# Optimization experiments

Measured on AMD Instinct MI355X. Metric: run time of the kernel, lower is better.

Reference implementation:

```python
import jax, jax.numpy as jnp
import numpy as np

B, L, D = 2, 2048, 1024
H, Z = 16, 64  # n_heads, head_dim


def setup_inputs() -> dict:
    key = jax.random.key(0)
    k1, k2, k3 = jax.random.split(key, 3)
    scale = 1.0 / np.sqrt(D)  # keep projections O(1) for numeric sanity
    x = jax.random.normal(k1, (B, L, D), dtype=jnp.float32)
    Wq = jax.random.normal(k2, (H, Z, D), dtype=jnp.float32) * scale
    Wk = jax.random.normal(k3, (H, Z, D), dtype=jnp.float32) * scale
    beta = jnp.ones((1,), dtype=jnp.float32) / jnp.sqrt(jnp.float32(Z))  # default beta = 1/sqrt(head_dim)
    return {"x": x, "Wq": Wq, "Wk": Wk, "beta": beta}


def _energy(x, Wq, Wk, beta):
    # x: (b, l, d); Wq/Wk: (h, z, d); beta: (1,)
    kp = jnp.einsum('bld,hzd->blhz', x, Wk)
    qp = jnp.einsum('bld,hzd->blhz', x, Wq)
    b0 = beta[0]
    # attention[b,h,q,k] = beta * <k_proj[b,q,h], q_proj[b,k,h]>  (faithful to original index order)
    att = b0 * jnp.einsum('bqhz,bkhz->bhqk', kp, qp)
    e = jax.nn.logsumexp(att, axis=-1)          # (b, h, q)
    e = e.sum(axis=-1).sum(axis=-1)             # (b,)
    return (-1.0 / b0) * e


def reference(x, Wq, Wk, beta):
    # value_and_grad: forward returns (energy, d(energy.sum)/dx)
    def esum(xx):
        return _energy(xx, Wq, Wk, beta).sum()
    en = _energy(x, Wq, Wk, beta)               # (b,)
    gx = jax.grad(esum)(x)                      # (b, l, d)
    return en, gx
```

## Files before the change

kernel.cpp:

```cpp
#include <hip/hip_runtime.h>
#include <math.h>

#define L 2048
#define D 1024
#define H 16
#define Z 64
#define HZ 1024

typedef __bf16 bf16x8 __attribute__((ext_vector_type(8)));
typedef float f32x4 __attribute__((ext_vector_type(4)));
typedef float f32x16 __attribute__((ext_vector_type(16)));

#if __has_builtin(__builtin_amdgcn_exp2f)
#define EXP2(x) __builtin_amdgcn_exp2f(x)
#else
#define EXP2(x) exp2f(x)
#endif

__device__ __forceinline__ void async_ld16(const void* g, void* l) {
  __builtin_amdgcn_global_load_lds(
      (const __attribute__((address_space(1))) uint32_t*)(uintptr_t)g,
      (__attribute__((address_space(3))) uint32_t*)(uint32_t)(uintptr_t)l,
      16, 0, 0);
}

template<int NPIECE>
__device__ __forceinline__ void stage_async(const __bf16* __restrict__ g,
                                            int gstride, char* lds, int tid) {
  const int l = tid & 63, w = tid >> 6;
#pragma unroll
  for (int it = 0; it < NPIECE; ++it) {
    const int region = it * 4 + w;
    const int r = ((region >> 1) << 4) + (l & 15);
    const int c = ((region & 1) << 2) + (l >> 4);
    async_ld16(g + (size_t)r * gstride + c * 8, lds + (region << 10));
  }
}

__device__ __forceinline__ bf16x8 rfrag(const char* lds, int row, int cc) {
  const int region = ((row >> 4) << 1) + (cc >> 2);
  const int slot = (row & 15) + ((cc & 3) << 4);
  return *(const bf16x8*)(lds + region * 1024 + slot * 16);
}

__global__ __launch_bounds__(256) void cvt_kernel(const float* __restrict__ s,
                                                  __bf16* __restrict__ d, int n4) {
  int i = blockIdx.x * 256 + threadIdx.x;
  if (i < n4) {
    float4 v = ((const float4*)s)[i];
    union { __bf16 h[4]; uint2 u; } o;
    o.h[0] = (__bf16)v.x; o.h[1] = (__bf16)v.y;
    o.h[2] = (__bf16)v.z; o.h[3] = (__bf16)v.w;
    ((uint2*)d)[i] = o.u;
  }
}

__global__ __launch_bounds__(256) void wt_kernel(
    const float* __restrict__ Wk, const float* __restrict__ Wq,
    __bf16* __restrict__ Wkb, __bf16* __restrict__ Wqb,
    __bf16* __restrict__ Wkt, __bf16* __restrict__ Wqt) {
  const float* W = blockIdx.z ? Wq : Wk;
  __bf16* Wb = blockIdx.z ? Wqb : Wkb;
  __bf16* Wt = blockIdx.z ? Wqt : Wkt;
  __shared__ __bf16 tile[64][65];
  const int r0 = blockIdx.y * 64, c0 = blockIdx.x * 64;
  const int c = threadIdx.x & 63, rb = threadIdx.x >> 6;
#pragma unroll
  for (int i = 0; i < 16; ++i) {
    int r = rb + i * 4;
    __bf16 v = (__bf16)W[(size_t)(r0 + r) * D + c0 + c];
    tile[r][c] = v;
    Wb[(size_t)(r0 + r) * D + c0 + c] = v;
  }
  __syncthreads();
#pragma unroll
  for (int i = 0; i < 16; ++i) {
    int r = rb + i * 4;
    Wt[(size_t)(c0 + r) * HZ + r0 + c] = tile[c][r];
  }
}

__device__ __forceinline__ int lperm(int mg) {
  const int off = mg & 15;
  return (mg & ~15) | (((off >> 2) & 1) << 3) | (((off >> 3) & 1) << 2);
}

__global__ __launch_bounds__(256, 2) void proj_kernel(
    const __bf16* __restrict__ xb, const __bf16* __restrict__ Wkb,
    const __bf16* __restrict__ Wqb, const float* __restrict__ beta_p,
    __bf16* __restrict__ kp, __bf16* __restrict__ qp,
    __bf16* __restrict__ kpt, __bf16* __restrict__ qpt) {
  const __bf16* __restrict__ Wb = blockIdx.z ? Wqb : Wkb;
  __bf16* __restrict__ outn = blockIdx.z ? qp : kp;
  __bf16* __restrict__ outt = blockIdx.z ? qpt : kpt;
  const int n0 = blockIdx.x * 128, m0 = blockIdx.y * 128;
  const int tid = threadIdx.x, l = tid & 63, w = tid >> 6;
  const int l31 = l & 31, hi = l >> 5;
  const int mh = w >> 1, nh = w & 1;
  const float ab = beta_p[0] * 1.44269504f;
  const float ssc = sqrtf(fabsf(ab));
  const float sc = blockIdx.z ? ssc : ((ab < 0.f) ? -ssc : ssc);
  __shared__ __align__(16) char sA[2][16384], sB[2][16384];

  f32x16 acc[2][2];
#pragma unroll
  for (int mi = 0; mi < 2; ++mi)
#pragma unroll
    for (int ni = 0; ni < 2; ++ni)
#pragma unroll
      for (int i = 0; i < 16; ++i) acc[mi][ni][i] = 0.f;

  const __bf16* __restrict__ Abase = xb + (size_t)m0 * D;
  const __bf16* __restrict__ Bbase = Wb + (size_t)n0 * D;
  stage_async<4>(Abase, D, sA[0], tid);
  stage_async<4>(Bbase, D, sB[0], tid);
  __syncthreads();

  for (int k = 0; k < 16; ++k) {
    const int cur = k & 1, nxt = cur ^ 1;
    if (k < 15) {
      stage_async<4>(Abase + (k + 1) * 64, D, sA[nxt], tid);
      stage_async<4>(Bbase + (k + 1) * 64, D, sB[nxt], tid);
    }
#pragma unroll
    for (int ks = 0; ks < 4; ++ks) {
      bf16x8 am[2], bn[2];
#pragma unroll
      for (int mi = 0; mi < 2; ++mi)
        am[mi] = rfrag(sA[cur], mh * 64 + mi * 32 + l31, 2 * ks + hi);
#pragma unroll
      for (int ni = 0; ni < 2; ++ni)
        bn[ni] = rfrag(sB[cur], nh * 64 + ni * 32 + l31, 2 * ks + hi);
#pragma unroll
      for (int mi = 0; mi < 2; ++mi)
#pragma unroll
        for (int ni = 0; ni < 2; ++ni)
          acc[mi][ni] = __builtin_amdgcn_mfma_f32_32x32x16_bf16(
              am[mi], bn[ni], acc[mi][ni], 0, 0, 0);
    }
    __syncthreads();
  }

  const int b = m0 >> 11;
  const int h = (n0 >> 6) + nh;
  const size_t bh = (size_t)b * H + h;
#pragma unroll
  for (int mi = 0; mi < 2; ++mi)
#pragma unroll
    for (int ni = 0; ni < 2; ++ni) {
      const int z = ni * 32 + l31;
#pragma unroll
      for (int rg = 0; rg < 4; ++rg) {
        const int mloc = mh * 64 + mi * 32 + 8 * rg + 4 * hi;
        const int mg = (m0 & (L - 1)) + mloc;
        union { __bf16 hh[4]; uint2 u; } pk;
#pragma unroll
        for (int j = 0; j < 4; ++j) {
          const float v = acc[mi][ni][4 * rg + j];
          pk.hh[j] = (__bf16)v;
          outn[(bh * L + mg + j) * Z + z] = (__bf16)(v * sc);
        }
        *(uint2*)(outt + (bh * Z + z) * L + lperm(mg)) = pk.u;
      }
    }
}

template<int MODE>
__global__ __launch_bounds__(256, 2) void grad_kernel(
    const __bf16* __restrict__ Rg, const __bf16* __restrict__ Sg,
    const __bf16* __restrict__ Tg,
    float* __restrict__ lse, __bf16* __restrict__ Gout) {
  const int bid = blockIdx.x;
  const int slot = bid >> 3;
  const int bh = (bid & 7) * 4 + (slot >> 4);
  const int qt = slot & 15;
  const int tid = threadIdx.x, l = tid & 63, w = tid >> 6;
  const int l31 = l & 31, hi = l >> 5;
  const int q0 = qt * 128 + w * 32;
  __shared__ __align__(16) char sS[3][8192], sT[3][8192];

  bf16x8 bres[4];
#pragma unroll
  for (int ks = 0; ks < 4; ++ks)
    bres[ks] = *(const bf16x8*)(
        Rg + ((size_t)bh * L + q0 + l31) * Z + ks * 16 + hi * 8);

  f32x16 pv[2];
#pragma unroll
  for (int zt = 0; zt < 2; ++zt)
#pragma unroll
    for (int i = 0; i < 16; ++i) pv[zt][i] = 0.f;
  float li = 0.f;

  const __bf16* __restrict__ Sbase = Sg + (size_t)bh * L * Z;
  const __bf16* __restrict__ Tbase = Tg + (size_t)bh * Z * L;

  stage_async<2>(Sbase, Z, sS[0], tid);
  stage_async<2>(Tbase, L, sT[0], tid);
  stage_async<2>(Sbase + (size_t)64 * Z, Z, sS[1], tid);
  stage_async<2>(Tbase + 64, L, sT[1], tid);
  asm volatile("s_waitcnt vmcnt(4)" ::: "memory");
  __builtin_amdgcn_s_barrier();

  const char* s0 = sS[0]; const char* s1 = sS[1]; char* s2 = sS[2];
  const char* t0 = sT[0]; const char* t1 = sT[1]; char* t2 = sT[2];

  for (int kt = 0; kt < 32; ++kt) {
    bf16x8 av[8], bt[8];
#pragma unroll
    for (int ks = 0; ks < 4; ++ks) {
      av[ks]     = rfrag(s0, l31,      2 * ks + hi);
      av[4 + ks] = rfrag(s0, 32 + l31, 2 * ks + hi);
      bt[2 * ks]     = rfrag(t0, l31,      2 * ks + hi);
      bt[2 * ks + 1] = rfrag(t0, 32 + l31, 2 * ks + hi);
    }
    if (kt < 30) {
      stage_async<2>(Sbase + (size_t)(kt + 2) * 64 * Z, Z, s2, tid);
      stage_async<2>(Tbase + (kt + 2) * 64, L, t2, tid);
    }
    f32x16 st[2];
#pragma unroll
    for (int i = 0; i < 16; ++i) { st[0][i] = 0.f; st[1][i] = 0.f; }
    __builtin_amdgcn_s_setprio(1);
#pragma unroll
    for (int ks = 0; ks < 4; ++ks) {
      st[0] = __builtin_amdgcn_mfma_f32_32x32x16_bf16(av[ks], bres[ks], st[0], 0, 0, 0);
      st[1] = __builtin_amdgcn_mfma_f32_32x32x16_bf16(av[4 + ks], bres[ks], st[1], 0, 0, 0);
    }
    __builtin_amdgcn_s_setprio(0);
    uint32_t P32[2][8];
    float lsn = 0.f;
#pragma unroll
    for (int nt = 0; nt < 2; ++nt)
#pragma unroll
      for (int i = 0; i < 8; ++i) {
        float e0 = EXP2(st[nt][2 * i]);
        float e1 = EXP2(st[nt][2 * i + 1]);
        if (MODE == 0) lsn += e0 + e1;
        union { __bf16 hh[2]; uint32_t u; } pk;
        pk.hh[0] = (__bf16)e0; pk.hh[1] = (__bf16)e1;
        P32[nt][i] = pk.u;
      }
    if (MODE == 0) li += lsn;
    __builtin_amdgcn_s_setprio(1);
#pragma unroll
    for (int kc = 0; kc < 4; ++kc) {
      union { uint32_t u[4]; bf16x8 v; } a;
#pragma unroll
      for (int i = 0; i < 4; ++i) a.u[i] = P32[kc >> 1][4 * (kc & 1) + i];
      pv[0] = __builtin_amdgcn_mfma_f32_32x32x16_bf16(a.v, bt[2 * kc], pv[0], 0, 0, 0);
      pv[1] = __builtin_amdgcn_mfma_f32_32x32x16_bf16(a.v, bt[2 * kc + 1], pv[1], 0, 0, 0);
    }
    __builtin_amdgcn_s_setprio(0);
    if (kt < 30) {
      asm volatile("s_waitcnt vmcnt(4)" ::: "memory");
      __builtin_amdgcn_s_barrier();
    } else if (kt == 30) {
      asm volatile("s_waitcnt vmcnt(0)" ::: "memory");
      __builtin_amdgcn_s_barrier();
    }
    const char* x;
    x = s0; s0 = s1; s1 = s2; s2 = (char*)x;
    x = t0; t0 = t1; t1 = t2; t2 = (char*)x;
  }

  if (MODE == 0) li += __shfl_xor(li, 32);
  const int b = bh >> 4, head = bh & (H - 1);
#pragma unroll
  for (int r = 0; r < 16; ++r) {
    const int qoff = (r & 3) + 8 * (r >> 2) + 4 * hi;
    float scl = 1.f;
    if (MODE == 0)
      scl = 1.f / __int_as_float(
                __builtin_amdgcn_ds_bpermute(4 * qoff, __float_as_int(li)));
    const size_t orow = ((size_t)b * L + q0 + qoff) * HZ + head * Z;
    Gout[orow + l31]      = (__bf16)(-pv[0][r] * scl);
    Gout[orow + 32 + l31] = (__bf16)(-pv[1][r] * scl);
  }
  if (MODE == 0 && hi == 0)
    lse[(size_t)bh * L + q0 + l31] = __logf(li);
}

__global__ __launch_bounds__(256) void kscale_kernel(__bf16* __restrict__ kpt,
                                                     const float* __restrict__ lse) {
  int idx = blockIdx.x * 256 + threadIdx.x;
  int row = idx >> 9;
  int pos4 = (idx & 511) << 2;
  int bh = row >> 6;
  int lbase = (pos4 & ~15) + (((pos4 >> 2) & 1) << 3) + (((pos4 >> 3) & 1) << 2);
  float4 ls = *(const float4*)(lse + (size_t)bh * L + lbase);
  __bf16* p = kpt + (size_t)row * L + pos4;
  union { __bf16 hh[4]; uint2 u; } v;
  v.u = *(uint2*)p;
  v.hh[0] = (__bf16)((float)v.hh[0] * __expf(-ls.x));
  v.hh[1] = (__bf16)((float)v.hh[1] * __expf(-ls.y));
  v.hh[2] = (__bf16)((float)v.hh[2] * __expf(-ls.z));
  v.hh[3] = (__bf16)((float)v.hh[3] * __expf(-ls.w));
  *(uint2*)p = v.u;
}

__global__ __launch_bounds__(256) void energy_kernel(
    const float* __restrict__ lse_ws, const float* __restrict__ beta_p,
    float* __restrict__ out) {
  const int b = blockIdx.x;
  const float* p = lse_ws + (size_t)b * H * L;
  float sum = 0.f;
  for (int i = threadIdx.x; i < H * L; i += 256) sum += p[i];
#pragma unroll
  for (int off = 1; off < 64; off <<= 1) sum += __shfl_xor(sum, off, 64);
  __shared__ float wsum[4];
  if ((threadIdx.x & 63) == 0) wsum[threadIdx.x >> 6] = sum;
  __syncthreads();
  if (threadIdx.x == 0)
    out[b] = -(wsum[0] + wsum[1] + wsum[2] + wsum[3]) / beta_p[0];
}

__global__ __launch_bounds__(256, 2) void gx_kernel(
    const __bf16* __restrict__ Gkp, const __bf16* __restrict__ Gqp,
    const __bf16* __restrict__ Wkt, const __bf16* __restrict__ Wqt,
    float* __restrict__ gx) {
  const int bid = blockIdx.x;
  const int xcd = bid & 7;
  const int nt_ = (bid >> 3) & 7;
  const int mg = bid >> 6;
  const int m0 = (xcd * 8 + mg) * 64;
  const int n0 = nt_ * 128;
  const int tid = threadIdx.x, l = tid & 63, w = tid >> 6;
  const int l31 = l & 31, hi = l >> 5;
  const int mh = w >> 1, nh = w & 1;
  __shared__ __align__(16) char sA[3][8192], sB[3][16384];

  f32x16 acc[2];
#pragma unroll
  for (int ni = 0; ni < 2; ++ni)
#pragma unroll
    for (int i = 0; i < 16; ++i) acc[ni][i] = 0.f;

  auto stageK = [&](int kn, char* a, char* b) {
    const __bf16* __restrict__ An = (kn < 16 ? Gkp : Gqp);
    const __bf16* __restrict__ Bn = (kn < 16 ? Wkt : Wqt);
    const int k0 = (kn & 15) * 64;
    stage_async<2>(An + (size_t)m0 * HZ + k0, HZ, a, tid);
    stage_async<4>(Bn + (size_t)n0 * HZ + k0, HZ, b, tid);
  };

  stageK(0, sA[0], sB[0]);
  stageK(1, sA[1], sB[1]);
  asm volatile("s_waitcnt vmcnt(6)" ::: "memory");
  __builtin_amdgcn_s_barrier();

  const char* a0 = sA[0]; const char* a1 = sA[1]; char* a2 = sA[2];
  const char* b0 = sB[0]; const char* b1 = sB[1]; char* b2 = sB[2];

  for (int kk = 0; kk < 32; ++kk) {
    if (kk < 30) stageK(kk + 2, a2, b2);
#pragma unroll
    for (int ks = 0; ks < 4; ++ks) {
      bf16x8 am, bn[2];
      am = rfrag(a0, mh * 32 + l31, 2 * ks + hi);
#pragma unroll
      for (int ni = 0; ni < 2; ++ni)
        bn[ni] = rfrag(b0, nh * 64 + ni * 32 + l31, 2 * ks + hi);
      __builtin_amdgcn_s_setprio(1);
#pragma unroll
      for (int ni = 0; ni < 2; ++ni)
        acc[ni] = __builtin_amdgcn_mfma_f32_32x32x16_bf16(
            am, bn[ni], acc[ni], 0, 0, 0);
      __builtin_amdgcn_s_setprio(0);
    }
    if (kk < 30) {
      asm volatile("s_waitcnt vmcnt(6)" ::: "memory");
      __builtin_amdgcn_s_barrier();
    } else if (kk == 30) {
      asm volatile("s_waitcnt vmcnt(0)" ::: "memory");
      __builtin_amdgcn_s_barrier();
    }
    const char* x;
    x = a0; a0 = a1; a1 = a2; a2 = (char*)x;
    x = b0; b0 = b1; b1 = b2; b2 = (char*)x;
  }
#pragma unroll
  for (int ni = 0; ni < 2; ++ni) {
    const int n = n0 + nh * 64 + ni * 32 + l31;
#pragma unroll
    for (int r = 0; r < 16; ++r) {
      const int m = m0 + mh * 32 + (r & 3) + 8 * (r >> 2) + 4 * hi;
      gx[(size_t)m * D + n] = acc[ni][r];
    }
  }
}

extern "C" void kernel_launch(void* const* d_in, const int* in_sizes, int n_in,
                              void* d_out, int out_size, void* d_ws, size_t ws_size,
                              hipStream_t stream) {
  const float* x    = (const float*)d_in[0];
  const float* Wq   = (const float*)d_in[1];
  const float* Wk   = (const float*)d_in[2];
  const float* beta = (const float*)d_in[3];
  float* out = (float*)d_out;

  char* ws = (char*)d_ws;
  __bf16* xb  = (__bf16*)(ws);
  __bf16* Wkb = (__bf16*)(ws + (8ull  << 20));
  __bf16* Wqb = (__bf16*)(ws + (10ull << 20));
  __bf16* Wkt = (__bf16*)(ws + (12ull << 20));
  __bf16* Wqt = (__bf16*)(ws + (14ull << 20));
  __bf16* kp  = (__bf16*)(ws + (16ull << 20));
  __bf16* qp  = (__bf16*)(ws + (24ull << 20));
  __bf16* kpt = (__bf16*)(ws + (32ull << 20));
  __bf16* qpt = (__bf16*)(ws + (40ull << 20));
  __bf16* Gkp = (__bf16*)(ws + (48ull << 20));
  __bf16* Gqp = (__bf16*)(ws + (56ull << 20));
  float*  lse = (float*)(ws + (64ull << 20));

  cvt_kernel<<<4096, 256, 0, stream>>>(x, xb, 1048576);
  wt_kernel<<<dim3(16, 16, 2), 256, 0, stream>>>(Wk, Wq, Wkb, Wqb, Wkt, Wqt);
  proj_kernel<<<dim3(8, 32, 2), 256, 0, stream>>>(xb, Wkb, Wqb, beta, kp, qp, kpt, qpt);
  grad_kernel<0><<<512, 256, 0, stream>>>(kp, qp, qpt, lse, Gkp);
  kscale_kernel<<<4096, 256, 0, stream>>>(kpt, lse);
  grad_kernel<1><<<512, 256, 0, stream>>>(qp, kp, kpt, lse, Gqp);
  energy_kernel<<<2, 256, 0, stream>>>(lse, beta, out);
  gx_kernel<<<512, 256, 0, stream>>>(Gkp, Gqp, Wkt, Wqt, out + 2);
}
```

Baseline: 284.6 us.

## Split key range across wave pairs with 64-row query tiles and LDS reduction

Restructures grad_kernel so each wave handles 64 query rows instead of 32, and the four waves split into two column groups, each covering half of the key sequence (split-K style). Each column group stages its own double-buffered S/T tiles, and at the end the partial PV accumulators and row sums are reduced through LDS. The larger query tile doubles reuse of each LDS fragment read per MFMA. In exchange it doubles accumulator register pressure, shortens the pipeline from triple to double buffering with a full vmcnt(0) wait each step, and adds a reduction phase in which half the waves sit idle.

```diff
diff --git a/kernel.cpp b/kernel.cpp
--- a/kernel.cpp
+++ b/kernel.cpp
@@ -31,6 +31,19 @@
 #pragma unroll
   for (int it = 0; it < NPIECE; ++it) {
     const int region = it * 4 + w;
+    const int r = ((region >> 1) << 4) + (l & 15);
+    const int c = ((region & 1) << 2) + (l >> 4);
+    async_ld16(g + (size_t)r * gstride + c * 8, lds + (region << 10));
+  }
+}
+
+template<int NPIECE, int NW>
+__device__ __forceinline__ void stage_asyncN(const __bf16* __restrict__ g,
+                                             int gstride, char* lds,
+                                             int l, int wl) {
+#pragma unroll
+  for (int it = 0; it < NPIECE; ++it) {
+    const int region = it * NW + wl;
     const int r = ((region >> 1) << 4) + (l & 15);
     const int c = ((region & 1) << 2) + (l >> 4);
     async_ld16(g + (size_t)r * gstride + c * 8, lds + (region << 10));
@@ -175,110 +188,169 @@
   const int bh = (bid & 7) * 4 + (slot >> 4);
   const int qt = slot & 15;
   const int tid = threadIdx.x, l = tid & 63, w = tid >> 6;
+  const int wq = w & 1, cg = w >> 1;
   const int l31 = l & 31, hi = l >> 5;
-  const int q0 = qt * 128 + w * 32;
-  __shared__ __align__(16) char sS[3][8192], sT[3][8192];
-
-  bf16x8 bres[4];
-#pragma unroll
-  for (int ks = 0; ks < 4; ++ks)
-    bres[ks] = *(const bf16x8*)(
+  const int q0 = qt * 128 + wq * 64;
+  __shared__ __align__(16) char sM[2][2][2][8192];
+
+  bf16x8 bres0[4], bres1[4];
+#pragma unroll
+  for (int ks = 0; ks < 4; ++ks) {
+    bres0[ks] = *(const bf16x8*)(
         Rg + ((size_t)bh * L + q0 + l31) * Z + ks * 16 + hi * 8);
-
-  f32x16 pv[2];
-#pragma unroll
-  for (int zt = 0; zt < 2; ++zt)
-#pragma unroll
-    for (int i = 0; i < 16; ++i) pv[zt][i] = 0.f;
-  float li = 0.f;
-
-  const __bf16* __restrict__ Sbase = Sg + (size_t)bh * L * Z;
-  const __bf16* __restrict__ Tbase = Tg + (size_t)bh * Z * L;
-
-  stage_async<2>(Sbase, Z, sS[0], tid);
-  stage_async<2>(Tbase, L, sT[0], tid);
-  stage_async<2>(Sbase + (size_t)64 * Z, Z, sS[1], tid);
-  stage_async<2>(Tbase + 64, L, sT[1], tid);
-  asm volatile("s_waitcnt vmcnt(4)" ::: "memory");
+    bres1[ks] = *(const bf16x8*)(
+        Rg + ((size_t)bh * L + q0 + 32 + l31) * Z + ks * 16 + hi * 8);
+  }
+
+  f32x16 pv00, pv01, pv10, pv11;
+#pragma unroll
+  for (int i = 0; i < 16; ++i) { pv00[i] = 0.f; pv01[i] = 0.f; pv10[i] = 0.f; pv11[i] = 0.f; }
+  float li0 = 0.f, li1 = 0.f;
+
+  const __bf16* __restrict__ Sbase = Sg + ((size_t)bh * L + cg * 1024) * Z;
+  const __bf16* __restrict__ Tbase = Tg + (size_t)bh * Z * L + cg * 1024;
+
+  stage_asyncN<4, 2>(Sbase, Z, sM[cg][0][0], l, wq);
+  stage_asyncN<4, 2>(Tbase, L, sM[cg][0][1], l, wq);
+  asm volatile("s_waitcnt vmcnt(0)" ::: "memory");
   __builtin_amdgcn_s_barrier();
 
-  const char* s0 = sS[0]; const char* s1 = sS[1]; char* s2 = sS[2];
-  const char* t0 = sT[0]; const char* t1 = sT[1]; char* t2 = sT[2];
-
-  for (int kt = 0; kt < 32; ++kt) {
+  for (int kt = 0; kt < 16; ++kt) {
+    const int cur = kt & 1, nxt = cur ^ 1;
+    if (kt < 15) {
+      stage_asyncN<4, 2>(Sbase + (size_t)(kt + 1) * 64 * Z, Z, sM[cg][nxt][0], l, wq);
+      stage_asyncN<4, 2>(Tbase + (kt + 1) * 64, L, sM[cg][nxt][1], l, wq);
+    }
     bf16x8 av[8], bt[8];
 #pragma unroll
     for (int ks = 0; ks < 4; ++ks) {
-      av[ks]     = rfrag(s0, l31,      2 * ks + hi);
-      av[4 + ks] = rfrag(s0, 32 + l31, 2 * ks + hi);
-      bt[2 * ks]     = rfrag(t0, l31,      2 * ks + hi);
-      bt[2 * ks + 1] = rfrag(t0, 32 + l31, 2 * ks + hi);
-    }
-    if (kt < 30) {
-      stage_async<2>(Sbase + (size_t)(kt + 2) * 64 * Z, Z, s2, tid);
-      stage_async<2>(Tbase + (kt + 2) * 64, L, t2, tid);
-    }
-    f32x16 st[2];
-#pragma unroll
-    for (int i = 0; i < 16; ++i) { st[0][i] = 0.f; st[1][i] = 0.f; }
+      av[ks]     = rfrag(sM[cg][cur][0], l31,      2 * ks + hi);
+      av[4 + ks] = rfrag(sM[cg][cur][0], 32 + l31, 2 * ks + hi);
+      bt[2 * ks]     = rfrag(sM[cg][cur][1], l31,      2 * ks + hi);
+      bt[2 * ks + 1] = rfrag(sM[cg][cur][1], 32 + l31, 2 * ks + hi);
+    }
+    uint32_t P0[2][8], P1[2][8];
+    {
+      f32x16 st0, st1;
+#pragma unroll
+      for (int i = 0; i < 16; ++i) { st0[i] = 0.f; st1[i] = 0.f; }
+      __builtin_amdgcn_s_setprio(1);
+#pragma unroll
+      for (int ks = 0; ks < 4; ++ks) {
+        st0 = __builtin_amdgcn_mfma_f32_32x32x16_bf16(av[ks], bres0[ks], st0, 0, 0, 0);
+        st1 = __builtin_amdgcn_mfma_f32_32x32x16_bf16(av[4 + ks], bres0[ks], st1, 0, 0, 0);
+      }
+      __builtin_amdgcn_s_setprio(0);
+      float lsn = 0.f;
+#pragma unroll
+      for (int i = 0; i < 8; ++i) {
+        float e0 = EXP2(st0[2 * i]), e1 = EXP2(st0[2 * i + 1]);
+        float e2 = EXP2(st1[2 * i]), e3 = EXP2(st1[2 * i + 1]);
+        if (MODE == 0) lsn += (e0 + e1) + (e2 + e3);
+        union { __bf16 hh[2]; uint32_t u; } pk;
+        pk.hh[0] = (__bf16)e0; pk.hh[1] = (__bf16)e1; P0[0][i] = pk.u;
+        pk.hh[0] = (__bf16)e2; pk.hh[1] = (__bf16)e3; P0[1][i] = pk.u;
+      }
+      if (MODE == 0) li0 += lsn;
+    }
+    {
+      f32x16 st0, st1;
+#pragma unroll
+      for (int i = 0; i < 16; ++i) { st0[i] = 0.f; st1[i] = 0.f; }
+      __builtin_amdgcn_s_setprio(1);
+#pragma unroll
+      for (int ks = 0; ks < 4; ++ks) {
+        st0 = __builtin_amdgcn_mfma_f32_32x32x16_bf16(av[ks], bres1[ks], st0, 0, 0, 0);
+        st1 = __builtin_amdgcn_mfma_f32_32x32x16_bf16(av[4 + ks], bres1[ks], st1, 0, 0, 0);
+      }
+      __builtin_amdgcn_s_setprio(0);
+      float lsn = 0.f;
+#pragma unroll
+      for (int i = 0; i < 8; ++i) {
+        float e0 = EXP2(st0[2 * i]), e1 = EXP2(st0[2 * i + 1]);
+        float e2 = EXP2(st1[2 * i]), e3 = EXP2(st1[2 * i + 1]);
+        if (MODE == 0) lsn += (e0 + e1) + (e2 + e3);
+        union { __bf16 hh[2]; uint32_t u; } pk;
+        pk.hh[0] = (__bf16)e0; pk.hh[1] = (__bf16)e1; P1[0][i] = pk.u;
+        pk.hh[0] = (__bf16)e2; pk.hh[1] = (__bf16)e3; P1[1][i] = pk.u;
+      }
+      if (MODE == 0) li1 += lsn;
+    }
     __builtin_amdgcn_s_setprio(1);
 #pragma unroll
-    for (int ks = 0; ks < 4; ++ks) {
-      st[0] = __builtin_amdgcn_mfma_f32_32x32x16_bf16(av[ks], bres[ks], st[0], 0, 0, 0);
-      st[1] = __builtin_amdgcn_mfma_f32_32x32x16_bf16(av[4 + ks], bres[ks], st[1], 0, 0, 0);
+    for (int kc = 0; kc < 4; ++kc) {
+      union { uint32_t u[4]; bf16x8 v; } a0, a1;
+#pragma unroll
+      for (int i = 0; i < 4; ++i) {
+        a0.u[i] = P0[kc >> 1][4 * (kc & 1) + i];
+        a1.u[i] = P1[kc >> 1][4 * (kc & 1) + i];
+      }
+      pv00 = __builtin_amdgcn_mfma_f32_32x32x16_bf16(a0.v, bt[2 * kc], pv00, 0, 0, 0);
+      pv01 = __builtin_amdgcn_mfma_f32_32x32x16_bf16(a0.v, bt[2 * kc + 1], pv01, 0, 0, 0);
+      pv10 = __builtin_amdgcn_mfma_f32_32x32x16_bf16(a1.v, bt[2 * kc], pv10, 0, 0, 0);
+      pv11 = __builtin_amdgcn_mfma_f32_32x32x16_bf16(a1.v, bt[2 * kc + 1], pv11, 0, 0, 0);
     }
     __builtin_amdgcn_s_setprio(0);
-    uint32_t P32[2][8];
-    float lsn = 0.f;
-#pragma unroll
-    for (int nt = 0; nt < 2; ++nt)
-#pragma unroll
-      for (int i = 0; i < 8; ++i) {
-        float e0 = EXP2(st[nt][2 * i]);
-        float e1 = EXP2(st[nt][2 * i + 1]);
-        if (MODE == 0) lsn += e0 + e1;
-        union { __bf16 hh[2]; uint32_t u; } pk;
-        pk.hh[0] = (__bf16)e0; pk.hh[1] = (__bf16)e1;
-        P32[nt][i] = pk.u;
-      }
-    if (MODE == 0) li += lsn;
-    __builtin_amdgcn_s_setprio(1);
-#pragma unroll
-    for (int kc = 0; kc < 4; ++kc) {
-      union { uint32_t u[4]; bf16x8 v; } a;
-#pragma unroll
-      for (int i = 0; i < 4; ++i) a.u[i] = P32[kc >> 1][4 * (kc & 1) + i];
-      pv[0] = __builtin_amdgcn_mfma_f32_32x32x16_bf16(a.v, bt[2 * kc], pv[0], 0, 0, 0);
-      pv[1] = __builtin_amdgcn_mfma_f32_32x32x16_bf16(a.v, bt[2 * kc + 1], pv[1], 0, 0, 0);
-    }
-    __builtin_amdgcn_s_setprio(0);
-    if (kt < 30) {
-      asm volatile("s_waitcnt vmcnt(4)" ::: "memory");
-      __builtin_amdgcn_s_barrier();
-    } else if (kt == 30) {
+    if (kt < 15) {
       asm volatile("s_waitcnt vmcnt(0)" ::: "memory");
       __builtin_amdgcn_s_barrier();
     }
-    const char* x;
-    x = s0; s0 = s1; s1 = s2; s2 = (char*)x;
-    x = t0; t0 = t1; t1 = t2; t2 = (char*)x;
-  }
-
-  if (MODE == 0) li += __shfl_xor(li, 32);
+  }
+
+  __syncthreads();
+  float* red = (float*)sM;
+  float* liRed = (float*)((char*)sM + 32768);
+  if (cg == 1) {
+#pragma unroll
+    for (int i = 0; i < 16; ++i) {
+      red[(wq * 64 +  0 + i) * 64 + l] = pv00[i];
+      red[(wq * 64 + 16 + i) * 64 + l] = pv01[i];
+      red[(wq * 64 + 32 + i) * 64 + l] = pv10[i];
+      red[(wq * 64 + 48 + i) * 64 + l] = pv11[i];
+    }
+    if (MODE == 0) {
+      liRed[wq * 128 + l] = li0;
+      liRed[wq * 128 + 64 + l] = li1;
+    }
+  }
+  __syncthreads();
+  if (cg == 1) return;
+#pragma unroll
+  for (int i = 0; i < 16; ++i) {
+    pv00[i] += red[(wq * 64 +  0 + i) * 64 + l];
+    pv01[i] += red[(wq * 64 + 16 + i) * 64 + l];
+    pv10[i] += red[(wq * 64 + 32 + i) * 64 + l];
+    pv11[i] += red[(wq * 64 + 48 + i) * 64 + l];
+  }
+  if (MODE == 0) {
+    li0 += liRed[wq * 128 + l];
+    li1 += liRed[wq * 128 + 64 + l];
+    li0 += __shfl_xor(li0, 32);
+    li1 += __shfl_xor(li1, 32);
+  }
+
   const int b = bh >> 4, head = bh & (H - 1);
 #pragma unroll
   for (int r = 0; r < 16; ++r) {
     const int qoff = (r & 3) + 8 * (r >> 2) + 4 * hi;
-    float scl = 1.f;
-    if (MODE == 0)
-      scl = 1.f / __int_as_float(
-                __builtin_amdgcn_ds_bpermute(4 * qoff, __float_as_int(li)));
-    const size_t orow = ((size_t)b * L + q0 + qoff) * HZ + head * Z;
-    Gout[orow + l31]      = (__bf16)(-pv[0][r] * scl);
-    Gout[orow + 32 + l31] = (__bf16)(-pv[1][r] * scl);
-  }
-  if (MODE == 0 && hi == 0)
-    lse[(size_t)bh * L + q0 + l31] = __logf(li);
+    float s0 = 1.f, s1 = 1.f;
+    if (MODE == 0) {
+      s0 = 1.f / __int_as_float(
+               __builtin_amdgcn_ds_bpermute(4 * qoff, __float_as_int(li0)));
+      s1 = 1.f / __int_as_float(
+               __builtin_amdgcn_ds_bpermute(4 * qoff, __float_as_int(li1)));
+    }
+    const size_t orow0 = ((size_t)b * L + q0 + qoff) * HZ + head * Z;
+    const size_t orow1 = ((size_t)b * L + q0 + 32 + qoff) * HZ + head * Z;
+    Gout[orow0 + l31]      = (__bf16)(-pv00[r] * s0);
+    Gout[orow0 + 32 + l31] = (__bf16)(-pv01[r] * s0);
+    Gout[orow1 + l31]      = (__bf16)(-pv10[r] * s1);
+    Gout[orow1 + 32 + l31] = (__bf16)(-pv11[r] * s1);
+  }
+  if (MODE == 0 && hi == 0) {
+    lse[(size_t)bh * L + q0 + l31] = __logf(li0);
+    lse[(size_t)bh * L + q0 + 32 + l31] = __logf(li1);
+  }
 }
 
 __global__ __launch_bounds__(256) void kscale_kernel(__bf16* __restrict__ kpt,
```

New measurement: 307.2 us. +8.0%, slower.
